# Performance work log

Hardware: AMD Instinct MI355X
Metric: run time of the kernel (lower is better)

Reference implementation:

```python
import jax, jax.numpy as jnp
import numpy as np

EMBED_DIM = 1024
NUM_HEADS = 16
HEAD_DIM = EMBED_DIM // NUM_HEADS
N, S = 4, 8192


def setup_inputs() -> dict:
    key = jax.random.key(0)
    ks = jax.random.split(key, 9)
    sc = 1.0 / np.sqrt(EMBED_DIM)
    d = {"x": jax.random.normal(ks[0], (N, S, EMBED_DIM), dtype=jnp.float32)}
    for i, name in enumerate(["Wq", "Wk", "Wv", "Wo"]):
        d[name] = jax.random.normal(ks[1 + i], (EMBED_DIM, EMBED_DIM), dtype=jnp.float32) * sc
    for i, name in enumerate(["bq", "bk", "bv", "bo"]):
        d[name] = jax.random.normal(ks[5 + i], (EMBED_DIM,), dtype=jnp.float32) * 0.01
    return d


def reference(x, Wq, Wk, Wv, Wo, bq, bk, bv, bo):
    n, s, e = x.shape
    # projections: nn.Linear => x @ W.T + b
    Q = x @ Wq.T + bq
    K = x @ Wk.T + bk
    V = x @ Wv.T + bv
    # (N, S, H, D) -> (N, H, S, D), matching torch .view().transpose(1, 2)
    Q = Q.reshape(n, s, NUM_HEADS, HEAD_DIM).transpose(0, 2, 1, 3)
    K = K.reshape(n, s, NUM_HEADS, HEAD_DIM).transpose(0, 2, 1, 3)
    V = V.reshape(n, s, NUM_HEADS, HEAD_DIM).transpose(0, 2, 1, 3)
    # Faithful to the original (buggy) einsum labeling: on (N,H,S,D) tensors
    # 'nqhd,nkhd->nhqk' attends OVER THE HEAD AXIS -> energy (N, S, H, H)
    energy = jnp.einsum('nqhd,nkhd->nhqk', Q, K)
    attention = jax.nn.softmax(energy / jnp.sqrt(jnp.float32(e)), axis=3)
    # out: (N, H, S, D), then reshaped as if (N, S, H*D) — exact original math
    out = jnp.einsum('nhql,nlhd->nqhd', attention, V).reshape(n, s, e)
    return out @ Wo.T + bo
```

## Files before the change

### kernel.cpp

```cpp
#include <hip/hip_runtime.h>
#include <cstdint>
#include <cstddef>

typedef unsigned short u16;
typedef __attribute__((ext_vector_type(8))) __bf16 bf16x8;
typedef __attribute__((ext_vector_type(4))) float floatx4;

typedef const __attribute__((address_space(1))) void* gptr_t;
typedef __attribute__((address_space(3))) void* lptr_t;

__device__ __forceinline__ u16 f2b(float f) {
    unsigned u = __builtin_bit_cast(unsigned, f);
    u += 0x7fffu + ((u >> 16) & 1u);
    return (u16)(u >> 16);
}

template <int N>
__device__ __forceinline__ float ror_add(float x) {
    int y = __builtin_amdgcn_update_dpp(0, __builtin_bit_cast(int, x), 0x120 + N, 0xF, 0xF, true);
    return x + __builtin_bit_cast(float, y);
}
template <int N>
__device__ __forceinline__ float ror_max(float x) {
    int y = __builtin_amdgcn_update_dpp(0, __builtin_bit_cast(int, x), 0x120 + N, 0xF, 0xF, true);
    return fmaxf(x, __builtin_bit_cast(float, y));
}

__global__ void cast_x(const float* __restrict__ in, u16* __restrict__ out, int n4) {
    const int stride = gridDim.x * blockDim.x;
    for (int i = blockIdx.x * blockDim.x + threadIdx.x; i < n4; i += stride) {
        const float4 v = ((const float4*)in)[i];
        ushort4 o;
        o.x = f2b(v.x); o.y = f2b(v.y); o.z = f2b(v.z); o.w = f2b(v.w);
        ((ushort4*)out)[i] = o;
    }
}

__global__ void cast_w(const float* __restrict__ Wq, const float* __restrict__ Wk,
                       const float* __restrict__ Wv, const float* __restrict__ Wo,
                       u16* __restrict__ Wqkv, u16* __restrict__ Wob) {
    const int stride = gridDim.x * blockDim.x;
    for (int i = blockIdx.x * blockDim.x + threadIdx.x; i < 1048576; i += stride) {
        const int which = i >> 18;
        const int local = i & 0x3FFFF;
        const float* src = which == 0 ? Wq : which == 1 ? Wk : which == 2 ? Wv : Wo;
        const float4 v = ((const float4*)src)[local];
        ushort4 o;
        o.x = f2b(v.x); o.y = f2b(v.y); o.z = f2b(v.z); o.w = f2b(v.w);
        ushort4* dst = which < 3 ? (ushort4*)Wqkv + which * 262144 + local
                                 : (ushort4*)Wob + local;
        *dst = o;
    }
}

template <bool OUT_BF16>
__device__ __forceinline__
void gemm_body(const u16* __restrict__ A, const u16* __restrict__ B,
               const float* __restrict__ b0, const float* __restrict__ b1,
               const float* __restrict__ b2, void* __restrict__ Cout,
               int N, int K)
{
    __shared__ u16 lA[128 * 32];
    __shared__ u16 lB[128 * 32];

    const int tid  = threadIdx.x;
    const int m0   = blockIdx.y * 128;
    const int n0   = blockIdx.x * 128;
    const int row  = tid >> 2;
    const int chk  = tid & 3;
    const int lane = tid & 63;
    const int wv   = tid >> 6;
    const int wm   = wv >> 1;
    const int wn   = wv & 1;
    const int lrow = lane & 15;
    const int quad = lane >> 4;

    const u16* gA0 = A + (size_t)(m0 + row) * K + chk * 8;
    const u16* gB0 = B + (size_t)(n0 + row) * K + chk * 8;
    u16* sA0 = lA + tid * 8;
    u16* sB0 = lB + tid * 8;

    const u16* pA = lA + (wm * 64 + lrow) * 32 + quad * 8;
    const u16* pB = lB + (wn * 64 + lrow) * 32 + quad * 8;

    const floatx4 fzero = {0.f, 0.f, 0.f, 0.f};
    floatx4 acc[4][4];
    #pragma unroll
    for (int i = 0; i < 4; i++)
        #pragma unroll
        for (int j = 0; j < 4; j++) acc[i][j] = fzero;

    const size_t rstride = (size_t)64 * K;

    for (int k0 = 0; k0 < K; k0 += 32) {
        __builtin_amdgcn_global_load_lds((gptr_t)(gA0 + k0),           (lptr_t)sA0,          16, 0, 0);
        __builtin_amdgcn_global_load_lds((gptr_t)(gA0 + rstride + k0), (lptr_t)(sA0 + 2048), 16, 0, 0);
        __builtin_amdgcn_global_load_lds((gptr_t)(gB0 + k0),           (lptr_t)sB0,          16, 0, 0);
        __builtin_amdgcn_global_load_lds((gptr_t)(gB0 + rstride + k0), (lptr_t)(sB0 + 2048), 16, 0, 0);
        __syncthreads();

        bf16x8 af[4], bfr[4];
        #pragma unroll
        for (int i = 0; i < 4; i++) {
            af[i]  = *(const bf16x8*)(pA + i * 512);
            bfr[i] = *(const bf16x8*)(pB + i * 512);
        }
        #pragma unroll
        for (int i = 0; i < 4; i++)
            #pragma unroll
            for (int j = 0; j < 4; j++)
                acc[i][j] = __builtin_amdgcn_mfma_f32_16x16x32_bf16(af[i], bfr[j], acc[i][j], 0, 0, 0);
        __syncthreads();
    }

    float bsv[4];
    #pragma unroll
    for (int j = 0; j < 4; j++) {
        const int n = n0 + wn * 64 + j * 16 + lrow;
        const float* bp = n < 1024 ? b0 : (n < 2048 ? b1 : b2);
        bsv[j] = bp[n & 1023];
    }

    #pragma unroll
    for (int i = 0; i < 4; i++) {
        const int mbase = m0 + wm * 64 + i * 16 + quad * 4;
        #pragma unroll
        for (int j = 0; j < 4; j++) {
            const int n = n0 + wn * 64 + j * 16 + lrow;
            #pragma unroll
            for (int r = 0; r < 4; r++) {
                const float v = acc[i][j][r] + bsv[j];
                const size_t idx = (size_t)(mbase + r) * N + n;
                if constexpr (OUT_BF16) ((u16*)Cout)[idx] = f2b(v);
                else                    ((float*)Cout)[idx] = v;
            }
        }
    }
}

__global__ __launch_bounds__(256, 2)
void gemm_qkv(const u16* __restrict__ A, const u16* __restrict__ B,
              const float* __restrict__ b0, const float* __restrict__ b1,
              const float* __restrict__ b2, u16* __restrict__ C, int N, int K)
{ gemm_body<true>(A, B, b0, b1, b2, (void*)C, N, K); }

__global__ __launch_bounds__(256, 2)
void gemm_out(const u16* __restrict__ A, const u16* __restrict__ B,
              const float* __restrict__ b0, float* __restrict__ C, int N, int K)
{ gemm_body<false>(A, B, b0, b0, b0, (void*)C, N, K); }

__global__ __launch_bounds__(256)
void attn_v3(const u16* __restrict__ QKV, u16* __restrict__ Z)
{
    __shared__ __align__(16) u16 sV[4][1024];
    __shared__ __align__(16) u16 sA[4][640];
    __shared__ __align__(16) u16 sY[16 * 1152];

    const int tid  = threadIdx.x;
    const int lane = tid & 63;
    const int wv   = tid >> 6;
    const int lrow = lane & 15;
    const int quad = lane >> 4;
    const int pp   = lane >> 3;
    const int cc   = lane & 7;

    #pragma unroll
    for (int i = 0; i < 4; i++) {
        const int idx = i * 64 + lane;
        sA[wv][(idx >> 4) * 40 + 16 + (idx & 15)] = 0;
    }

    const int tgrp = blockIdx.x * 16;
    const int nb   = tgrp >> 13;
    const int sg   = (tgrp & 8191) >> 4;

    const floatx4 fzero = {0.f, 0.f, 0.f, 0.f};

    for (int tt = 0; tt < 4; tt++) {
        const int t = wv * 4 + tt;
        const u16* base = QKV + (size_t)(tgrp + t) * 3072;

        const bf16x8 q0 = *(const bf16x8*)(base + lrow * 64      + quad * 8);
        const bf16x8 q1 = *(const bf16x8*)(base + lrow * 64 + 32 + quad * 8);
        const bf16x8 k0 = *(const bf16x8*)(base + 1024 + lrow * 64      + quad * 8);
        const bf16x8 k1 = *(const bf16x8*)(base + 1024 + lrow * 64 + 32 + quad * 8);

        const u16* V = base + 2048;
        const bf16x8 va = *(const bf16x8*)(V + (2 * pp)     * 64 + cc * 8);
        const bf16x8 vb = *(const bf16x8*)(V + (2 * pp + 1) * 64 + cc * 8);
        #pragma unroll
        for (int s = 0; s < 8; s++) {
            const unsigned pv = (unsigned)__builtin_bit_cast(u16, (__bf16)va[s]) |
                                ((unsigned)__builtin_bit_cast(u16, (__bf16)vb[s]) << 16);
            *(unsigned*)&sV[wv][(s * 8 + cc) * 16 + 2 * pp] = pv;
        }

        floatx4 e = fzero;
        e = __builtin_amdgcn_mfma_f32_16x16x32_bf16(q0, k0, e, 0, 0, 0);
        e = __builtin_amdgcn_mfma_f32_16x16x32_bf16(q1, k1, e, 0, 0, 0);

        #pragma unroll
        for (int r = 0; r < 4; r++) {
            const float xv = e[r] * 0.03125f;
            float mx = xv;
            mx = ror_max<1>(mx); mx = ror_max<2>(mx);
            mx = ror_max<4>(mx); mx = ror_max<8>(mx);
            const float p = __expf(xv - mx);
            float s = p;
            s = ror_add<1>(s); s = ror_add<2>(s);
            s = ror_add<4>(s); s = ror_add<8>(s);
            sA[wv][(quad * 4 + r) * 40 + lrow] = f2b(p * __builtin_amdgcn_rcpf(s));
        }

        const bf16x8 af = *(const bf16x8*)&sA[wv][lrow * 40 + quad * 8];

        bf16x8 bfr[4];
        #pragma unroll
        for (int j = 0; j < 4; j++)
            #pragma unroll
            for (int jj = 0; jj < 8; jj++)
                bfr[j][jj] = __builtin_bit_cast(__bf16, (u16)0);
        if (quad < 2) {
            #pragma unroll
            for (int j = 0; j < 4; j++) {
                const int pr = (lrow & 7) * 8 + j * 2 + (lrow >> 3);
                bfr[j] = *(const bf16x8*)&sV[wv][pr * 16 + quad * 8];
            }
        }

        #pragma unroll
        for (int j = 0; j < 4; j++) {
            const floatx4 y = __builtin_amdgcn_mfma_f32_16x16x32_bf16(af, bfr[j], fzero, 0, 0, 0);
            #pragma unroll
            for (int r = 0; r < 4; r++)
                sY[t * 1152 + (quad * 4 + r) * 72 + j * 16 + lrow] = f2b(y[r]);
        }
    }

    __syncthreads();

    const int h   = tid >> 4;
    const int pos = tid & 15;
    u16* zrow = Z + (size_t)(nb * 8192 + h * 512 + sg) * 1024;
    #pragma unroll
    for (int it = 0; it < 8; it++) {
        const int c16 = it * 16 + pos;
        const int t = c16 >> 3, dc = c16 & 7;
        const uint4 v = *(const uint4*)&sY[t * 1152 + h * 72 + dc * 8];
        *(uint4*)(zrow + c16 * 8) = v;
    }
}

extern "C" void kernel_launch(void* const* d_in, const int* in_sizes, int n_in,
                              void* d_out, int out_size, void* d_ws, size_t ws_size,
                              hipStream_t stream)
{
    (void)in_sizes; (void)n_in; (void)out_size;
    const float* x  = (const float*)d_in[0];
    const float* Wq = (const float*)d_in[1];
    const float* Wk = (const float*)d_in[2];
    const float* Wv = (const float*)d_in[3];
    const float* Wo = (const float*)d_in[4];
    const float* bq = (const float*)d_in[5];
    const float* bk = (const float*)d_in[6];
    const float* bv = (const float*)d_in[7];
    const float* bo = (const float*)d_in[8];

    const size_t Mtot = 32768;
    char* ws = (char*)d_ws;
    u16* Xbf  = (u16*)ws;
    u16* Wqkv = (u16*)(ws + (64ull << 20));
    u16* Wob  = (u16*)(ws + (64ull << 20) + (6ull << 20));
    char* dyn = ws + (72ull << 20);
    const size_t fixed = (72ull << 20);

    int c = 4;
    for (int cc = 1; cc <= 4; cc <<= 1) {
        size_t Rr = Mtot / cc;
        if (fixed + Rr * 3072 * 2 + Rr * 1024 * 2 <= ws_size) { c = cc; break; }
    }
    const size_t R = Mtot / c;
    u16* QKV = (u16*)dyn;
    u16* Zb  = (u16*)(dyn + R * 3072 * 2);

    cast_x<<<dim3(4096), dim3(256), 0, stream>>>(x, Xbf, (int)(Mtot * 1024 / 4));
    cast_w<<<dim3(1024), dim3(256), 0, stream>>>(Wq, Wk, Wv, Wo, Wqkv, Wob);

    for (int ci = 0; ci < c; ci++) {
        const u16* Ab   = Xbf + (size_t)ci * R * 1024;
        float*     outp = (float*)d_out + (size_t)ci * R * 1024;
        gemm_qkv<<<dim3(24, (unsigned)(R / 128)), dim3(256), 0, stream>>>(Ab, Wqkv, bq, bk, bv, QKV, 3072, 1024);
        attn_v3<<<dim3((unsigned)(R / 16)), dim3(256), 0, stream>>>(QKV, Zb);
        gemm_out<<<dim3(8, (unsigned)(R / 128)), dim3(256), 0, stream>>>(Zb, Wob, bo, outp, 1024, 1024);
    }
}
```

Measured before the change: 621.3 us.

## Replace GEMMs with 256x256 eight-wave pipelined kernel using swizzled LDS

Replaces the simple 128x128 single-buffered GEMM used for the QKV and output projections with a 256x256-tile, 512-thread kernel. It double-buffers LDS via async global-to-LDS loads interleaved with MFMA phases, uses XOR-swizzled LDS addressing and priority raising, and remaps workgroup IDs for L2 locality. The aim is to hide global load latency, cut barrier stalls and increase data reuse per tile. The code is far more complex, hardcodes K=1024 and requires R divisible by 256 as a power of two.

After: 573.3 us. -7.7%, faster.

```diff
diff --git a/kernel.cpp b/kernel.cpp
--- a/kernel.cpp
+++ b/kernel.cpp
@@ -53,83 +53,243 @@
     }
 }
 
+
+#define MFMA16(va, vb, vc) __builtin_amdgcn_mfma_f32_16x16x32_bf16((va), (vb), (vc), 0, 0, 0)
+#define PH_BAR()  __builtin_amdgcn_s_barrier()
+#define PH_LGKM() asm volatile("s_waitcnt lgkmcnt(0)" ::: "memory")
+
 template <bool OUT_BF16>
-__device__ __forceinline__
-void gemm_body(const u16* __restrict__ A, const u16* __restrict__ B,
-               const float* __restrict__ b0, const float* __restrict__ b1,
-               const float* __restrict__ b2, void* __restrict__ Cout,
-               int N, int K)
+__global__ __launch_bounds__(512, 2)
+void gemm8(const u16* __restrict__ A, const u16* __restrict__ B,
+           const float* __restrict__ b0, const float* __restrict__ b1,
+           const float* __restrict__ b2, void* __restrict__ Cout,
+           int N, int mshift)
 {
-    __shared__ u16 lA[128 * 32];
-    __shared__ u16 lB[128 * 32];
+    __shared__ __align__(16) u16 lds[65536];
+
+    const int nwg = gridDim.x;
+    const int bid = blockIdx.x;
+    const int swz = (bid & 7) * (nwg >> 3) + (bid >> 3);
+    const int ntile = swz >> mshift;
+    const int mtile = swz & ((1 << mshift) - 1);
+    const int bm0 = mtile << 8;
+    const int bn0 = ntile << 8;
 
     const int tid  = threadIdx.x;
-    const int m0   = blockIdx.y * 128;
-    const int n0   = blockIdx.x * 128;
-    const int row  = tid >> 2;
-    const int chk  = tid & 3;
     const int lane = tid & 63;
     const int wv   = tid >> 6;
-    const int wm   = wv >> 1;
-    const int wn   = wv & 1;
+    const int wm   = wv >> 2;
+    const int wn   = wv & 3;
     const int lrow = lane & 15;
     const int quad = lane >> 4;
 
-    const u16* gA0 = A + (size_t)(m0 + row) * K + chk * 8;
-    const u16* gB0 = B + (size_t)(n0 + row) * K + chk * 8;
-    u16* sA0 = lA + tid * 8;
-    u16* sB0 = lB + tid * 8;
-
-    const u16* pA = lA + (wm * 64 + lrow) * 32 + quad * 8;
-    const u16* pB = lB + (wn * 64 + lrow) * 32 + quad * 8;
-
-    const floatx4 fzero = {0.f, 0.f, 0.f, 0.f};
-    floatx4 acc[4][4];
+    const int srow = lane >> 2;
+    const int scol = ((lane & 3) * 8) ^ (((lane >> 5) & 1) << 4);
+    const u16* aS = A + (size_t)(bm0 + wv * 16 + srow) * 1024 + scol;
+    const u16* bS = B + (size_t)(bn0 + wv * 16 + srow) * 1024 + scol;
+    u16* aD = lds +         wv * 1024 + lane * 8;
+    u16* bD = lds + 32768 + wv * 1024 + lane * 8;
+
+    const int laneSw = lrow * 32 + ((quad * 8) ^ ((lrow >> 3) << 4));
+    const u16* pA = lds +         wm * 8192 + laneSw;
+    const u16* pB = lds + 32768 + wn * 4096 + laneSw;
+
+    auto stage = [&](const u16* src, u16* dst, int kt, int half, int buf) {
+        const u16* s = src + (size_t)half * 131072 + kt * 64;
+        u16* d = dst + buf * 16384 + half * 8192;
+        __builtin_amdgcn_global_load_lds((gptr_t)s,        (lptr_t)d,         16, 0, 0);
+        __builtin_amdgcn_global_load_lds((gptr_t)(s + 32), (lptr_t)(d + 512), 16, 0, 0);
+    };
+
+    stage(aS, aD, 0, 0, 0);
+    stage(aS, aD, 0, 1, 0);
+    stage(bS, bD, 0, 0, 0);
+    stage(bS, bD, 0, 1, 0);
+    asm volatile("" ::: "memory");
+    stage(bS, bD, 1, 0, 1);
+    stage(bS, bD, 1, 1, 1);
+    asm volatile("s_waitcnt vmcnt(4)" ::: "memory");
+    PH_BAR();
+
+    const floatx4 fz = {0.f, 0.f, 0.f, 0.f};
+    floatx4 acc[8][4];
     #pragma unroll
-    for (int i = 0; i < 4; i++)
-        #pragma unroll
-        for (int j = 0; j < 4; j++) acc[i][j] = fzero;
-
-    const size_t rstride = (size_t)64 * K;
-
-    for (int k0 = 0; k0 < K; k0 += 32) {
-        __builtin_amdgcn_global_load_lds((gptr_t)(gA0 + k0),           (lptr_t)sA0,          16, 0, 0);
-        __builtin_amdgcn_global_load_lds((gptr_t)(gA0 + rstride + k0), (lptr_t)(sA0 + 2048), 16, 0, 0);
-        __builtin_amdgcn_global_load_lds((gptr_t)(gB0 + k0),           (lptr_t)sB0,          16, 0, 0);
-        __builtin_amdgcn_global_load_lds((gptr_t)(gB0 + rstride + k0), (lptr_t)(sB0 + 2048), 16, 0, 0);
-        __syncthreads();
-
-        bf16x8 af[4], bfr[4];
-        #pragma unroll
-        for (int i = 0; i < 4; i++) {
-            af[i]  = *(const bf16x8*)(pA + i * 512);
-            bfr[i] = *(const bf16x8*)(pB + i * 512);
-        }
-        #pragma unroll
-        for (int i = 0; i < 4; i++)
-            #pragma unroll
-            for (int j = 0; j < 4; j++)
-                acc[i][j] = __builtin_amdgcn_mfma_f32_16x16x32_bf16(af[i], bfr[j], acc[i][j], 0, 0, 0);
-        __syncthreads();
+    for (int i = 0; i < 8; ++i)
+        #pragma unroll
+        for (int t = 0; t < 4; ++t) acc[i][t] = fz;
+
+    bf16x8 a[4][2], p0[2][2], p1[2][2];
+
+    for (int j = 0; j < 8; ++j) {
+        const int kt1 = 2 * j + 1;
+        const int kt2 = 2 * j + 2;
+        const int kt3 = 2 * j + 3;
+        const bool more = (j < 7);
+
+        #pragma unroll
+        for (int i = 0; i < 4; ++i) {
+            a[i][0] = *(const bf16x8*)(pA + i * 1024);
+            a[i][1] = *(const bf16x8*)(pA + i * 1024 + 512);
+        }
+        #pragma unroll
+        for (int t = 0; t < 2; ++t) {
+            p0[t][0] = *(const bf16x8*)(pB + t * 1024);
+            p0[t][1] = *(const bf16x8*)(pB + t * 1024 + 512);
+        }
+        stage(aS, aD, kt1, 0, 1);
+        PH_BAR(); PH_LGKM();
+        __builtin_amdgcn_s_setprio(1);
+        #pragma unroll
+        for (int i = 0; i < 4; ++i)
+            #pragma unroll
+            for (int t = 0; t < 2; ++t) {
+                acc[i][t] = MFMA16(a[i][0], p0[t][0], acc[i][t]);
+                acc[i][t] = MFMA16(a[i][1], p0[t][1], acc[i][t]);
+            }
+        __builtin_amdgcn_s_setprio(0);
+        PH_BAR();
+
+        #pragma unroll
+        for (int t = 0; t < 2; ++t) {
+            p1[t][0] = *(const bf16x8*)(pB + 2048 + t * 1024);
+            p1[t][1] = *(const bf16x8*)(pB + 2048 + t * 1024 + 512);
+        }
+        stage(aS, aD, kt1, 1, 1);
+        PH_BAR(); PH_LGKM();
+        __builtin_amdgcn_s_setprio(1);
+        #pragma unroll
+        for (int i = 0; i < 4; ++i)
+            #pragma unroll
+            for (int t = 0; t < 2; ++t) {
+                acc[i][2 + t] = MFMA16(a[i][0], p1[t][0], acc[i][2 + t]);
+                acc[i][2 + t] = MFMA16(a[i][1], p1[t][1], acc[i][2 + t]);
+            }
+        __builtin_amdgcn_s_setprio(0);
+        PH_BAR();
+
+        #pragma unroll
+        for (int i = 0; i < 4; ++i) {
+            a[i][0] = *(const bf16x8*)(pA + 4096 + i * 1024);
+            a[i][1] = *(const bf16x8*)(pA + 4096 + i * 1024 + 512);
+        }
+        if (more) stage(bS, bD, kt2, 0, 0);
+        PH_BAR(); PH_LGKM();
+        __builtin_amdgcn_s_setprio(1);
+        #pragma unroll
+        for (int i = 0; i < 4; ++i)
+            #pragma unroll
+            for (int t = 0; t < 2; ++t) {
+                acc[4 + i][2 + t] = MFMA16(a[i][0], p1[t][0], acc[4 + i][2 + t]);
+                acc[4 + i][2 + t] = MFMA16(a[i][1], p1[t][1], acc[4 + i][2 + t]);
+            }
+        __builtin_amdgcn_s_setprio(0);
+        PH_BAR();
+
+        if (more) stage(bS, bD, kt2, 1, 0);
+        PH_BAR();
+        __builtin_amdgcn_s_setprio(1);
+        #pragma unroll
+        for (int i = 0; i < 4; ++i)
+            #pragma unroll
+            for (int t = 0; t < 2; ++t) {
+                acc[4 + i][t] = MFMA16(a[i][0], p0[t][0], acc[4 + i][t]);
+                acc[4 + i][t] = MFMA16(a[i][1], p0[t][1], acc[4 + i][t]);
+            }
+        __builtin_amdgcn_s_setprio(0);
+        if (more) asm volatile("s_waitcnt vmcnt(4)" ::: "memory");
+        else      asm volatile("s_waitcnt vmcnt(0)" ::: "memory");
+        PH_BAR();
+
+        #pragma unroll
+        for (int i = 0; i < 4; ++i) {
+            a[i][0] = *(const bf16x8*)(pA + 16384 + i * 1024);
+            a[i][1] = *(const bf16x8*)(pA + 16384 + i * 1024 + 512);
+        }
+        #pragma unroll
+        for (int t = 0; t < 2; ++t) {
+            p0[t][0] = *(const bf16x8*)(pB + 16384 + t * 1024);
+            p0[t][1] = *(const bf16x8*)(pB + 16384 + t * 1024 + 512);
+        }
+        if (more) stage(aS, aD, kt2, 0, 0);
+        PH_BAR(); PH_LGKM();
+        __builtin_amdgcn_s_setprio(1);
+        #pragma unroll
+        for (int i = 0; i < 4; ++i)
+            #pragma unroll
+            for (int t = 0; t < 2; ++t) {
+                acc[i][t] = MFMA16(a[i][0], p0[t][0], acc[i][t]);
+                acc[i][t] = MFMA16(a[i][1], p0[t][1], acc[i][t]);
+            }
+        __builtin_amdgcn_s_setprio(0);
+        PH_BAR();
+
+        #pragma unroll
+        for (int t = 0; t < 2; ++t) {
+            p1[t][0] = *(const bf16x8*)(pB + 16384 + 2048 + t * 1024);
+            p1[t][1] = *(const bf16x8*)(pB + 16384 + 2048 + t * 1024 + 512);
+        }
+        if (more) stage(aS, aD, kt2, 1, 0);
+        PH_BAR(); PH_LGKM();
+        __builtin_amdgcn_s_setprio(1);
+        #pragma unroll
+        for (int i = 0; i < 4; ++i)
+            #pragma unroll
+            for (int t = 0; t < 2; ++t) {
+                acc[i][2 + t] = MFMA16(a[i][0], p1[t][0], acc[i][2 + t]);
+                acc[i][2 + t] = MFMA16(a[i][1], p1[t][1], acc[i][2 + t]);
+            }
+        __builtin_amdgcn_s_setprio(0);
+        PH_BAR();
+
+        #pragma unroll
+        for (int i = 0; i < 4; ++i) {
+            a[i][0] = *(const bf16x8*)(pA + 16384 + 4096 + i * 1024);
+            a[i][1] = *(const bf16x8*)(pA + 16384 + 4096 + i * 1024 + 512);
+        }
+        if (more) stage(bS, bD, kt3, 0, 1);
+        PH_BAR(); PH_LGKM();
+        __builtin_amdgcn_s_setprio(1);
+        #pragma unroll
+        for (int i = 0; i < 4; ++i)
+            #pragma unroll
+            for (int t = 0; t < 2; ++t) {
+                acc[4 + i][2 + t] = MFMA16(a[i][0], p1[t][0], acc[4 + i][2 + t]);
+                acc[4 + i][2 + t] = MFMA16(a[i][1], p1[t][1], acc[4 + i][2 + t]);
+            }
+        __builtin_amdgcn_s_setprio(0);
+        PH_BAR();
+
+        if (more) stage(bS, bD, kt3, 1, 1);
+        PH_BAR();
+        __builtin_amdgcn_s_setprio(1);
+        #pragma unroll
+        for (int i = 0; i < 4; ++i)
+            #pragma unroll
+            for (int t = 0; t < 2; ++t) {
+                acc[4 + i][t] = MFMA16(a[i][0], p0[t][0], acc[4 + i][t]);
+                acc[4 + i][t] = MFMA16(a[i][1], p0[t][1], acc[4 + i][t]);
+            }
+        __builtin_amdgcn_s_setprio(0);
+        asm volatile("s_waitcnt vmcnt(4)" ::: "memory");
+        PH_BAR();
     }
 
     float bsv[4];
     #pragma unroll
-    for (int j = 0; j < 4; j++) {
-        const int n = n0 + wn * 64 + j * 16 + lrow;
+    for (int t = 0; t < 4; ++t) {
+        const int n = bn0 + wn * 64 + t * 16 + lrow;
         const float* bp = n < 1024 ? b0 : (n < 2048 ? b1 : b2);
-        bsv[j] = bp[n & 1023];
-    }
-
+        bsv[t] = bp[n & 1023];
+    }
     #pragma unroll
-    for (int i = 0; i < 4; i++) {
-        const int mbase = m0 + wm * 64 + i * 16 + quad * 4;
-        #pragma unroll
-        for (int j = 0; j < 4; j++) {
-            const int n = n0 + wn * 64 + j * 16 + lrow;
-            #pragma unroll
-            for (int r = 0; r < 4; r++) {
-                const float v = acc[i][j][r] + bsv[j];
+    for (int i = 0; i < 8; ++i) {
+        const int mbase = bm0 + wm * 128 + i * 16 + quad * 4;
+        #pragma unroll
+        for (int t = 0; t < 4; ++t) {
+            const int n = bn0 + wn * 64 + t * 16 + lrow;
+            #pragma unroll
+            for (int r = 0; r < 4; ++r) {
+                const float v = acc[i][t][r] + bsv[t];
                 const size_t idx = (size_t)(mbase + r) * N + n;
                 if constexpr (OUT_BF16) ((u16*)Cout)[idx] = f2b(v);
                 else                    ((float*)Cout)[idx] = v;
@@ -137,17 +297,6 @@
         }
     }
 }
-
-__global__ __launch_bounds__(256, 2)
-void gemm_qkv(const u16* __restrict__ A, const u16* __restrict__ B,
-              const float* __restrict__ b0, const float* __restrict__ b1,
-              const float* __restrict__ b2, u16* __restrict__ C, int N, int K)
-{ gemm_body<true>(A, B, b0, b1, b2, (void*)C, N, K); }
-
-__global__ __launch_bounds__(256, 2)
-void gemm_out(const u16* __restrict__ A, const u16* __restrict__ B,
-              const float* __restrict__ b0, float* __restrict__ C, int N, int K)
-{ gemm_body<false>(A, B, b0, b0, b0, (void*)C, N, K); }
 
 __global__ __launch_bounds__(256)
 void attn_v3(const u16* __restrict__ QKV, u16* __restrict__ Z)
@@ -286,11 +435,14 @@
     cast_x<<<dim3(4096), dim3(256), 0, stream>>>(x, Xbf, (int)(Mtot * 1024 / 4));
     cast_w<<<dim3(1024), dim3(256), 0, stream>>>(Wq, Wk, Wv, Wo, Wqkv, Wob);
 
+    const int mt  = (int)(R >> 8);
+    const int msh = __builtin_ctz((unsigned)mt);
+
     for (int ci = 0; ci < c; ci++) {
         const u16* Ab   = Xbf + (size_t)ci * R * 1024;
         float*     outp = (float*)d_out + (size_t)ci * R * 1024;
-        gemm_qkv<<<dim3(24, (unsigned)(R / 128)), dim3(256), 0, stream>>>(Ab, Wqkv, bq, bk, bv, QKV, 3072, 1024);
+        gemm8<true><<<dim3(mt * 12), dim3(512), 0, stream>>>(Ab, Wqkv, bq, bk, bv, QKV, 3072, msh);
         attn_v3<<<dim3((unsigned)(R / 16)), dim3(256), 0, stream>>>(QKV, Zb);
-        gemm_out<<<dim3(8, (unsigned)(R / 128)), dim3(256), 0, stream>>>(Zb, Wob, bo, outp, 1024, 1024);
-    }
-}
+        gemm8<false><<<dim3(mt * 4), dim3(512), 0, stream>>>(Zb, Wob, bo, bo, bo, outp, 1024, msh);
+    }
+}
```
